# Kernel tuning notes

Hardware: AMD Instinct MI355X
Metric: run time of the kernel (lower is better)

The kernel has to match this reference:

```python
import jax, jax.numpy as jnp
import numpy as np

NUM_EDGES = 131072  # number of hyperedges (segments)


def setup_inputs() -> dict:
    key = jax.random.key(0)
    k_x, k_idx, k_w1, k_w2 = jax.random.split(key, 4)
    NNZ, D_IN, D_HID, D_OUT = 2097152, 128, 512, 128
    x = jax.random.normal(k_x, (NNZ, D_IN), dtype=jnp.float32)
    hyperedge_index = jax.random.randint(k_idx, (2, NNZ), 0, NUM_EDGES).astype(jnp.int64)
    # MLP params (num_layers=2: Linear(d_in,hid) -> ReLU -> Linear(hid,d_out))
    W1 = jax.random.normal(k_w1, (D_IN, D_HID), dtype=jnp.float32) / np.sqrt(D_IN)
    b1 = jnp.zeros((D_HID,), dtype=jnp.float32)
    W2 = jax.random.normal(k_w2, (D_HID, D_OUT), dtype=jnp.float32) / np.sqrt(D_HID)
    b2 = jnp.zeros((D_OUT,), dtype=jnp.float32)
    return {"x": x, "hyperedge_index": hyperedge_index, "W1": W1, "b1": b1, "W2": W2, "b2": b2}


def reference(x, hyperedge_index, W1, b1, W2, b2):
    seg = hyperedge_index[1]  # hyperedge id per incidence entry
    # scatter_mean over dim 0: segmented sum / count (empty segments -> 0)
    sums = jax.ops.segment_sum(x, seg, num_segments=NUM_EDGES)          # [E, d_in]
    cnt = jax.ops.segment_sum(jnp.ones((x.shape[0],), x.dtype), seg, num_segments=NUM_EDGES)
    mean = sums / jnp.maximum(cnt, 1.0)[:, None]                        # [E, d_in]
    # MLP: Linear -> ReLU -> Linear (norm_type='None', dropout inactive)
    h = jax.nn.relu(mean @ W1 + b1)
    return h @ W2 + b2
```

## Files before the change

kernel.cpp:

```cpp
#include <hip/hip_runtime.h>

#define E_EDGES 131072
#define D_IN 128
#define D_HID 512
#define D_OUT 128

typedef __bf16 bf16x8 __attribute__((ext_vector_type(8)));
typedef float f32x4 __attribute__((ext_vector_type(4)));

__device__ __forceinline__ unsigned short f2bf(float f) {
    unsigned int u = __float_as_uint(f);
    unsigned int r = (u + 0x7FFFu + ((u >> 16) & 1u)) >> 16;
    return (unsigned short)r;
}

__global__ void zero_kernel(int* __restrict__ cnt) {
    int i = blockIdx.x * blockDim.x + threadIdx.x;
    if (i < E_EDGES) cnt[i] = 0;
}

__global__ void hist_kernel(const int* __restrict__ seg, int* __restrict__ cnt, int nnz) {
    int i = blockIdx.x * blockDim.x + threadIdx.x;
    int stride = gridDim.x * blockDim.x;
    for (; i < nnz; i += stride) {
        atomicAdd(&cnt[seg[i]], 1);
    }
}

__global__ void scan_kernel(const int* __restrict__ cnt, int* __restrict__ off,
                            int* __restrict__ cur) {
    __shared__ int lds[1024];
    const int t = threadIdx.x;
    const int base = t * 128;
    int s = 0;
    for (int j = 0; j < 128; ++j) s += cnt[base + j];
    lds[t] = s;
    __syncthreads();
    for (int d = 1; d < 1024; d <<= 1) {
        int v = (t >= d) ? lds[t - d] : 0;
        __syncthreads();
        lds[t] += v;
        __syncthreads();
    }
    int run = lds[t] - s;
    for (int j = 0; j < 128; ++j) {
        off[base + j] = run;
        cur[base + j] = run;
        run += cnt[base + j];
    }
    if (t == 1023) off[E_EDGES] = run;
}

__global__ void fill_kernel(const int* __restrict__ seg, int* __restrict__ cur,
                            int* __restrict__ csr, int nnz) {
    int i = blockIdx.x * blockDim.x + threadIdx.x;
    int stride = gridDim.x * blockDim.x;
    for (; i < nnz; i += stride) {
        int p = atomicAdd(&cur[seg[i]], 1);
        csr[p] = i;
    }
}

__global__ void convw_kernel(const float* __restrict__ W1, const float* __restrict__ W2,
                             unsigned short* __restrict__ w1b, unsigned short* __restrict__ w2b) {
    int i = blockIdx.x * blockDim.x + threadIdx.x;
    if (i < D_IN * D_HID) {
        int n = i >> 7, k = i & 127;
        w1b[i] = f2bf(W1[(size_t)k * D_HID + n]);
    } else {
        int i2 = i - D_IN * D_HID;
        int n = i2 >> 9, k = i2 & 511;
        w2b[i2] = f2bf(W2[(size_t)k * D_OUT + n]);
    }
}

__global__ __launch_bounds__(256) void fused_kernel(
    const float* __restrict__ x, const int* __restrict__ csr,
    const int* __restrict__ off, const unsigned short* __restrict__ w1b,
    const unsigned short* __restrict__ w2b, const float* __restrict__ b1,
    const float* __restrict__ b2, float* __restrict__ out)
{
    __shared__ unsigned short mean_lds[64 * 128];
    __shared__ unsigned short hslice[4][16 * 32];

    const int tid  = threadIdx.x;
    const int lane = tid & 63;
    const int w    = tid >> 6;
    const int tile = blockIdx.x;
    const int row0 = w * 16;

    for (int el = 0; el < 16; ++el) {
        const int row = row0 + el;
        const int eid = tile * 64 + row;
        const int beg = off[eid], end = off[eid + 1];
        const int n = end - beg;
        const int* ce = csr + beg;
        float s0x = 0.f, s0y = 0.f, s1x = 0.f, s1y = 0.f;
        float s2x = 0.f, s2y = 0.f, s3x = 0.f, s3y = 0.f;
        int j = 0;
        for (; j + 4 <= n; j += 4) {
            int i0 = ce[j], i1 = ce[j + 1], i2 = ce[j + 2], i3 = ce[j + 3];
            float2 v0 = *((const float2*)(x + (size_t)i0 * D_IN) + lane);
            float2 v1 = *((const float2*)(x + (size_t)i1 * D_IN) + lane);
            float2 v2 = *((const float2*)(x + (size_t)i2 * D_IN) + lane);
            float2 v3 = *((const float2*)(x + (size_t)i3 * D_IN) + lane);
            s0x += v0.x; s0y += v0.y; s1x += v1.x; s1y += v1.y;
            s2x += v2.x; s2y += v2.y; s3x += v3.x; s3y += v3.y;
        }
        for (; j < n; ++j) {
            int i0 = ce[j];
            float2 v0 = *((const float2*)(x + (size_t)i0 * D_IN) + lane);
            s0x += v0.x; s0y += v0.y;
        }
        float sx = (s0x + s1x) + (s2x + s3x);
        float sy = (s0y + s1y) + (s2y + s3y);
        const float scale = 1.0f / (float)(n > 0 ? n : 1);
        sx *= scale; sy *= scale;
        unsigned int byte = ((unsigned)(row * 256 + lane * 4)) ^ ((unsigned)(row & 7) << 4);
        *(unsigned int*)((char*)mean_lds + byte) =
            (unsigned)f2bf(sx) | ((unsigned)f2bf(sy) << 16);
    }

    const int lrow = lane & 15;
    const int lgrp = lane >> 4;

    bf16x8 afrag[4];
#pragma unroll
    for (int kk = 0; kk < 4; ++kk) {
        int row = row0 + lrow;
        unsigned int byte = ((unsigned)(row * 256 + kk * 64 + lgrp * 16)) ^ ((unsigned)(row & 7) << 4);
        afrag[kk] = *(const bf16x8*)((const char*)mean_lds + byte);
    }

    const f32x4 fzero = {0.f, 0.f, 0.f, 0.f};
    f32x4 acc2[8];
#pragma unroll
    for (int t = 0; t < 8; ++t) acc2[t] = fzero;

    unsigned short* hs = &hslice[w][0];

    for (int ntp = 0; ntp < 16; ++ntp) {
#pragma unroll
        for (int half = 0; half < 2; ++half) {
            const int nt = ntp * 2 + half;
            f32x4 acc = fzero;
#pragma unroll
            for (int kk = 0; kk < 4; ++kk) {
                const bf16x8 b = *(const bf16x8*)(w1b + (size_t)(nt * 16 + lrow) * 128 + kk * 32 + lgrp * 8);
                acc = __builtin_amdgcn_mfma_f32_16x16x32_bf16(afrag[kk], b, acc, 0, 0, 0);
            }
            const int hcol = nt * 16 + lrow;
            const float bias = b1[hcol];
#pragma unroll
            for (int r = 0; r < 4; ++r) {
                float v = acc[r] + bias;
                v = fmaxf(v, 0.f);
                const int rowD = lgrp * 4 + r;
                const int klocal = half * 16 + lrow;
                unsigned int byte = ((unsigned)(rowD * 64 + klocal * 2)) ^ ((unsigned)(rowD & 3) << 4);
                *(unsigned short*)((char*)hs + byte) = f2bf(v);
            }
        }
        {
            unsigned int byte = ((unsigned)(lrow * 64 + lgrp * 16)) ^ ((unsigned)(lrow & 3) << 4);
            const bf16x8 a2 = *(const bf16x8*)((const char*)hs + byte);
#pragma unroll
            for (int nt2 = 0; nt2 < 8; ++nt2) {
                const bf16x8 b = *(const bf16x8*)(w2b + (size_t)(nt2 * 16 + lrow) * 512 + ntp * 32 + lgrp * 8);
                acc2[nt2] = __builtin_amdgcn_mfma_f32_16x16x32_bf16(a2, b, acc2[nt2], 0, 0, 0);
            }
        }
    }

#pragma unroll
    for (int nt2 = 0; nt2 < 8; ++nt2) {
        const int col = nt2 * 16 + lrow;
        const float bias = b2[col];
#pragma unroll
        for (int r = 0; r < 4; ++r) {
            const int row = tile * 64 + row0 + lgrp * 4 + r;
            out[(size_t)row * 128 + col] = acc2[nt2][r] + bias;
        }
    }
}

extern "C" void kernel_launch(void* const* d_in, const int* in_sizes, int n_in,
                              void* d_out, int out_size, void* d_ws, size_t ws_size,
                              hipStream_t stream)
{
    const float* x  = (const float*)d_in[0];
    const int* hyper = (const int*)d_in[1];
    const float* W1 = (const float*)d_in[2];
    const float* b1 = (const float*)d_in[3];
    const float* W2 = (const float*)d_in[4];
    const float* b2 = (const float*)d_in[5];
    const int nnz = in_sizes[0] / D_IN;
    const int* seg = hyper + nnz;

    char* ws = (char*)d_ws;
    int* cnt = (int*)(ws + 0x000000);
    int* off = (int*)(ws + 0x080000);
    int* cur = (int*)(ws + 0x100100);
    int* csr = (int*)(ws + 0x180100);
    unsigned short* w1b = (unsigned short*)(ws + 0x980100);
    unsigned short* w2b = (unsigned short*)(ws + 0x9A0100);
    float* out = (float*)d_out;

    hipLaunchKernelGGL(zero_kernel, dim3(E_EDGES / 256), dim3(256), 0, stream, cnt);
    hipLaunchKernelGGL(hist_kernel, dim3(2048), dim3(256), 0, stream, seg, cnt, nnz);
    hipLaunchKernelGGL(scan_kernel, dim3(1), dim3(1024), 0, stream, cnt, off, cur);
    hipLaunchKernelGGL(fill_kernel, dim3(2048), dim3(256), 0, stream, seg, cur, csr, nnz);
    hipLaunchKernelGGL(convw_kernel, dim3((D_IN * D_HID + D_HID * D_OUT) / 256), dim3(256), 0,
                       stream, W1, W2, w1b, w2b);
    hipLaunchKernelGGL(fused_kernel, dim3(E_EDGES / 64), dim3(256), 0, stream,
                       x, csr, off, w1b, w2b, b1, b2, out);
}
```

Before: 882.0 us.

## Parallelize CSR scan and widen gather loads with int4/f32x4 vectorization

Replaces the single-block serial prefix scan with a three-stage block-sum, block-prefix and per-block scan across many blocks. Histogram and fill kernels now read segment ids as int4 and do four atomics per thread. The segment-mean gather uses 16-byte loads with each half-wavefront handling a different incidence row, combined via a cross-half shuffle, and segment offsets are loaded once per wave and broadcast by shuffle. This aims to cut the serialized scan latency and improve memory-level parallelism in the gather, at the cost of more kernel launches and a slightly more complex tail loop.

```diff
diff --git a/kernel.cpp b/kernel.cpp
--- a/kernel.cpp
+++ b/kernel.cpp
@@ -16,48 +16,86 @@
 
 __global__ void zero_kernel(int* __restrict__ cnt) {
     int i = blockIdx.x * blockDim.x + threadIdx.x;
-    if (i < E_EDGES) cnt[i] = 0;
+    ((int4*)cnt)[i] = make_int4(0, 0, 0, 0);
 }
 
 __global__ void hist_kernel(const int* __restrict__ seg, int* __restrict__ cnt, int nnz) {
     int i = blockIdx.x * blockDim.x + threadIdx.x;
-    int stride = gridDim.x * blockDim.x;
-    for (; i < nnz; i += stride) {
-        atomicAdd(&cnt[seg[i]], 1);
-    }
-}
-
-__global__ void scan_kernel(const int* __restrict__ cnt, int* __restrict__ off,
-                            int* __restrict__ cur) {
-    __shared__ int lds[1024];
-    const int t = threadIdx.x;
-    const int base = t * 128;
-    int s = 0;
-    for (int j = 0; j < 128; ++j) s += cnt[base + j];
-    lds[t] = s;
+    if (i * 4 < nnz) {
+        int4 s = ((const int4*)seg)[i];
+        atomicAdd(&cnt[s.x], 1);
+        atomicAdd(&cnt[s.y], 1);
+        atomicAdd(&cnt[s.z], 1);
+        atomicAdd(&cnt[s.w], 1);
+    }
+}
+
+__global__ void blocksum_kernel(const int* __restrict__ cnt, int* __restrict__ bsum) {
+    __shared__ int wsum[4];
+    const int b = blockIdx.x, t = threadIdx.x;
+    int4 c = ((const int4*)cnt)[b * 256 + t];
+    int s = c.x + c.y + c.z + c.w;
+    for (int d = 32; d; d >>= 1) s += __shfl_down(s, d);
+    if ((t & 63) == 0) wsum[t >> 6] = s;
     __syncthreads();
-    for (int d = 1; d < 1024; d <<= 1) {
-        int v = (t >= d) ? lds[t - d] : 0;
-        __syncthreads();
-        lds[t] += v;
-        __syncthreads();
-    }
-    int run = lds[t] - s;
-    for (int j = 0; j < 128; ++j) {
-        off[base + j] = run;
-        cur[base + j] = run;
-        run += cnt[base + j];
-    }
-    if (t == 1023) off[E_EDGES] = run;
+    if (t == 0) bsum[b] = wsum[0] + wsum[1] + wsum[2] + wsum[3];
+}
+
+__global__ void bscan_kernel(const int* __restrict__ bsum, int* __restrict__ bpre,
+                             int* __restrict__ off_last) {
+    const int l = threadIdx.x;
+    int a = bsum[2 * l], b = bsum[2 * l + 1];
+    int s = a + b;
+    for (int d = 1; d < 64; d <<= 1) {
+        int u = __shfl_up(s, d);
+        if (l >= d) s += u;
+    }
+    int excl = s - (a + b);
+    bpre[2 * l] = excl;
+    bpre[2 * l + 1] = excl + a;
+    if (l == 63) off_last[0] = s;
+}
+
+__global__ void scan2_kernel(const int* __restrict__ cnt, const int* __restrict__ bpre,
+                             int* __restrict__ off, int* __restrict__ cur) {
+    __shared__ int wsum[4];
+    const int b = blockIdx.x, t = threadIdx.x;
+    const int gid = b * 256 + t;
+    int4 c = ((const int4*)cnt)[gid];
+    const int s = c.x + c.y + c.z + c.w;
+    const int lane = t & 63, w = t >> 6;
+    int incl = s;
+    for (int d = 1; d < 64; d <<= 1) {
+        int u = __shfl_up(incl, d);
+        if (lane >= d) incl += u;
+    }
+    if (lane == 63) wsum[w] = incl;
+    __syncthreads();
+    int woff = 0;
+    for (int i = 0; i < w; ++i) woff += wsum[i];
+    const int base = bpre[b] + woff + (incl - s);
+    int4 o;
+    o.x = base;
+    o.y = base + c.x;
+    o.z = base + c.x + c.y;
+    o.w = base + c.x + c.y + c.z;
+    ((int4*)off)[gid] = o;
+    ((int4*)cur)[gid] = o;
 }
 
 __global__ void fill_kernel(const int* __restrict__ seg, int* __restrict__ cur,
                             int* __restrict__ csr, int nnz) {
     int i = blockIdx.x * blockDim.x + threadIdx.x;
-    int stride = gridDim.x * blockDim.x;
-    for (; i < nnz; i += stride) {
-        int p = atomicAdd(&cur[seg[i]], 1);
-        csr[p] = i;
+    if (i * 4 < nnz) {
+        int4 s = ((const int4*)seg)[i];
+        int p0 = atomicAdd(&cur[s.x], 1);
+        int p1 = atomicAdd(&cur[s.y], 1);
+        int p2 = atomicAdd(&cur[s.z], 1);
+        int p3 = atomicAdd(&cur[s.w], 1);
+        csr[p0] = i * 4;
+        csr[p1] = i * 4 + 1;
+        csr[p2] = i * 4 + 2;
+        csr[p3] = i * 4 + 3;
     }
 }
 
@@ -89,36 +127,51 @@
     const int tile = blockIdx.x;
     const int row0 = w * 16;
 
+    const int c  = lane & 31;
+    const int rr = lane >> 5;
+    const char* xb = (const char*)x + c * 16;
+
+    int oreg = off[tile * 64 + row0 + (lane < 17 ? lane : 16)];
+
     for (int el = 0; el < 16; ++el) {
         const int row = row0 + el;
-        const int eid = tile * 64 + row;
-        const int beg = off[eid], end = off[eid + 1];
+        const int beg = __shfl(oreg, el);
+        const int end = __shfl(oreg, el + 1);
         const int n = end - beg;
         const int* ce = csr + beg;
-        float s0x = 0.f, s0y = 0.f, s1x = 0.f, s1y = 0.f;
-        float s2x = 0.f, s2y = 0.f, s3x = 0.f, s3y = 0.f;
+        f32x4 a0 = {0.f, 0.f, 0.f, 0.f}, a1 = a0, a2 = a0, a3 = a0;
         int j = 0;
-        for (; j + 4 <= n; j += 4) {
-            int i0 = ce[j], i1 = ce[j + 1], i2 = ce[j + 2], i3 = ce[j + 3];
-            float2 v0 = *((const float2*)(x + (size_t)i0 * D_IN) + lane);
-            float2 v1 = *((const float2*)(x + (size_t)i1 * D_IN) + lane);
-            float2 v2 = *((const float2*)(x + (size_t)i2 * D_IN) + lane);
-            float2 v3 = *((const float2*)(x + (size_t)i3 * D_IN) + lane);
-            s0x += v0.x; s0y += v0.y; s1x += v1.x; s1y += v1.y;
-            s2x += v2.x; s2y += v2.y; s3x += v3.x; s3y += v3.y;
-        }
-        for (; j < n; ++j) {
-            int i0 = ce[j];
-            float2 v0 = *((const float2*)(x + (size_t)i0 * D_IN) + lane);
-            s0x += v0.x; s0y += v0.y;
-        }
-        float sx = (s0x + s1x) + (s2x + s3x);
-        float sy = (s0y + s1y) + (s2y + s3y);
+        for (; j + 8 <= n; j += 8) {
+            int i0 = ce[j + 0 + rr];
+            int i1 = ce[j + 2 + rr];
+            int i2 = ce[j + 4 + rr];
+            int i3 = ce[j + 6 + rr];
+            f32x4 v0 = *(const f32x4*)(xb + (size_t)i0 * 512);
+            f32x4 v1 = *(const f32x4*)(xb + (size_t)i1 * 512);
+            f32x4 v2 = *(const f32x4*)(xb + (size_t)i2 * 512);
+            f32x4 v3 = *(const f32x4*)(xb + (size_t)i3 * 512);
+            a0 += v0; a1 += v1; a2 += v2; a3 += v3;
+        }
+        for (; j < n; j += 2) {
+            const int jr = j + rr;
+            const bool valid = jr < n;
+            int idx = ce[valid ? jr : n - 1];
+            f32x4 v = *(const f32x4*)(xb + (size_t)idx * 512);
+            if (valid) a0 += v;
+        }
+        f32x4 tot = (a0 + a1) + (a2 + a3);
+        tot[0] += __shfl_xor(tot[0], 32);
+        tot[1] += __shfl_xor(tot[1], 32);
+        tot[2] += __shfl_xor(tot[2], 32);
+        tot[3] += __shfl_xor(tot[3], 32);
         const float scale = 1.0f / (float)(n > 0 ? n : 1);
-        sx *= scale; sy *= scale;
-        unsigned int byte = ((unsigned)(row * 256 + lane * 4)) ^ ((unsigned)(row & 7) << 4);
-        *(unsigned int*)((char*)mean_lds + byte) =
-            (unsigned)f2bf(sx) | ((unsigned)f2bf(sy) << 16);
+        if (lane < 32) {
+            unsigned int d0 = (unsigned)f2bf(tot[0] * scale) | ((unsigned)f2bf(tot[1] * scale) << 16);
+            unsigned int d1 = (unsigned)f2bf(tot[2] * scale) | ((unsigned)f2bf(tot[3] * scale) << 16);
+            unsigned int byte = ((unsigned)(row * 256 + c * 8)) ^ ((unsigned)(row & 7) << 4);
+            uint2* p = (uint2*)((char*)mean_lds + byte);
+            *p = make_uint2(d0, d1);
+        }
     }
 
     const int lrow = lane & 15;
@@ -198,18 +251,22 @@
     const int* seg = hyper + nnz;
 
     char* ws = (char*)d_ws;
-    int* cnt = (int*)(ws + 0x000000);
-    int* off = (int*)(ws + 0x080000);
-    int* cur = (int*)(ws + 0x100100);
-    int* csr = (int*)(ws + 0x180100);
+    int* cnt  = (int*)(ws + 0x000000);
+    int* off  = (int*)(ws + 0x080000);
+    int* cur  = (int*)(ws + 0x100100);
+    int* csr  = (int*)(ws + 0x180100);
     unsigned short* w1b = (unsigned short*)(ws + 0x980100);
     unsigned short* w2b = (unsigned short*)(ws + 0x9A0100);
+    int* bsum = (int*)(ws + 0x9C0100);
+    int* bpre = (int*)(ws + 0x9C0300);
     float* out = (float*)d_out;
 
-    hipLaunchKernelGGL(zero_kernel, dim3(E_EDGES / 256), dim3(256), 0, stream, cnt);
-    hipLaunchKernelGGL(hist_kernel, dim3(2048), dim3(256), 0, stream, seg, cnt, nnz);
-    hipLaunchKernelGGL(scan_kernel, dim3(1), dim3(1024), 0, stream, cnt, off, cur);
-    hipLaunchKernelGGL(fill_kernel, dim3(2048), dim3(256), 0, stream, seg, cur, csr, nnz);
+    hipLaunchKernelGGL(zero_kernel, dim3(128), dim3(256), 0, stream, cnt);
+    hipLaunchKernelGGL(hist_kernel, dim3(nnz / 1024), dim3(256), 0, stream, seg, cnt, nnz);
+    hipLaunchKernelGGL(blocksum_kernel, dim3(128), dim3(256), 0, stream, cnt, bsum);
+    hipLaunchKernelGGL(bscan_kernel, dim3(1), dim3(64), 0, stream, bsum, bpre, off + E_EDGES);
+    hipLaunchKernelGGL(scan2_kernel, dim3(128), dim3(256), 0, stream, cnt, bpre, off, cur);
+    hipLaunchKernelGGL(fill_kernel, dim3(nnz / 1024), dim3(256), 0, stream, seg, cur, csr, nnz);
     hipLaunchKernelGGL(convw_kernel, dim3((D_IN * D_HID + D_HID * D_OUT) / 256), dim3(256), 0,
                        stream, W1, W2, w1b, w2b);
     hipLaunchKernelGGL(fused_kernel, dim3(E_EDGES / 64), dim3(256), 0, stream,
```

Measured after the change: 775.1 us. 12.1% less time.
